# Performance work log

Hardware: AMD Instinct MI355X
Metric: run time of the kernel (lower is better)

Reference implementation:

```python
import jax, jax.numpy as jnp
import numpy as np

B, L, D, A = 4, 4096, 256, 64  # batch, seq_len, n_embd, att_size

def setup_inputs() -> dict:
    key = jax.random.key(0)
    kx, kq, kk, kv = jax.random.split(key, 4)
    x = jax.random.normal(kx, (B, L, D), dtype=jnp.float32)
    # torch nn.Linear(n_embd, att_size) weight is [att_size, n_embd]; we store transposed [D, A]
    s = 1.0 / np.sqrt(D)
    Wq = jax.random.normal(kq, (D, A), dtype=jnp.float32) * s
    Wk = jax.random.normal(kk, (D, A), dtype=jnp.float32) * s
    Wv = jax.random.normal(kv, (D, A), dtype=jnp.float32) * s
    return {"x": x, "Wq": Wq, "Wk": Wk, "Wv": Wv}

def reference(x, Wq, Wk, Wv):
    # q,k,v: [B,L,A]
    q = jnp.einsum('bld,da->bla', x, Wq)
    k = jnp.einsum('bld,da->bla', x, Wk)
    v = jnp.einsum('bld,da->bla', x, Wv)
    # NOTE: original module does NOT scale by 1/sqrt(att_size)
    scores = jnp.einsum('bqa,bka->bqk', q, k)  # [B,L,L]
    Lq = x.shape[1]
    causal = jnp.tril(jnp.ones((Lq, Lq), dtype=bool))
    scores = jnp.where(causal, scores, -jnp.inf)
    weights = jax.nn.softmax(scores, axis=-1)
    # dropout is identity in eval mode
    out = jnp.einsum('bqk,bka->bqa', weights, v)  # [B,L,A]
    return out
```

## Files before the change

### kernel.cpp

```cpp
#include <hip/hip_runtime.h>
#include <math.h>

#define B_ 4
#define L_ 4096
#define D_ 256
#define A_ 64
#define M_ (B_*L_)

typedef _Float16 half4 __attribute__((ext_vector_type(4)));
typedef _Float16 half8 __attribute__((ext_vector_type(8)));
typedef __attribute__((ext_vector_type(4))) float floatx4;

__device__ __forceinline__ unsigned short f2h_(float f) {
    _Float16 h = (_Float16)f;
    return __builtin_bit_cast(unsigned short, h);
}

__global__ __launch_bounds__(256) void wconv_kernel(
    const float* __restrict__ Wq, const float* __restrict__ Wk,
    const float* __restrict__ Wv, unsigned short* __restrict__ wt)
{
    const int w = blockIdx.x, t = threadIdx.x;
    const float* W = (w == 0) ? Wq : (w == 1) ? Wk : Wv;
    unsigned short* o = wt + w * A_ * D_;
    const float scale = (w == 0) ? 1.44269504f : 1.0f;
    __shared__ float T[A_ * 260];
    #pragma unroll
    for (int p = 0; p < 16; ++p) {
        int idx = p * 256 + t;
        int d = idx >> 4, a4 = (idx & 15) * 4;
        float4 v = *(const float4*)(W + d * A_ + a4);
        T[(a4 + 0) * 260 + d] = v.x * scale;
        T[(a4 + 1) * 260 + d] = v.y * scale;
        T[(a4 + 2) * 260 + d] = v.z * scale;
        T[(a4 + 3) * 260 + d] = v.w * scale;
    }
    __syncthreads();
    const int a = t >> 2, d0 = (t & 3) * 64;
    #pragma unroll
    for (int i = 0; i < 16; ++i) {
        float4 v = *(const float4*)(&T[a * 260 + d0 + 4 * i]);
        ushort4 s;
        s.x = f2h_(v.x); s.y = f2h_(v.y); s.z = f2h_(v.z); s.w = f2h_(v.w);
        *(ushort4*)(o + a * D_ + d0 + 4 * i) = s;
    }
}

__global__ __launch_bounds__(384) void proj_kernel(
    const float* __restrict__ x,
    const unsigned short* __restrict__ wt,
    unsigned short* __restrict__ qo,
    unsigned short* __restrict__ ko,
    unsigned short* __restrict__ vto)
{
    __shared__ __align__(16) unsigned short Xh[32 * 264];
    __shared__ __align__(16) unsigned short Cst[6 * 1536];
    const int t = threadIdx.x, m0 = blockIdx.x * 32;

    #pragma unroll
    for (int p = 0; p < 6; ++p) {
        int idx = p * 384 + t;
        if (idx < 2048) {
            int row = idx >> 6, col = (idx & 63) * 4;
            float4 v = *(const float4*)(x + (size_t)(m0 + row) * D_ + col);
            ushort4 s;
            s.x = f2h_(v.x); s.y = f2h_(v.y); s.z = f2h_(v.z); s.w = f2h_(v.w);
            *(ushort4*)(Xh + row * 264 + col) = s;
        }
    }
    __syncthreads();

    const int wid = t >> 6, lane = t & 63, c = lane & 15, g = lane >> 4;
    const int w = wid >> 1, mt = wid & 1;

    half8 xa[8];
    #pragma unroll
    for (int s = 0; s < 8; ++s)
        xa[s] = *(const half8*)(Xh + (16 * mt + c) * 264 + 32 * s + 8 * g);

    const unsigned short* wsrc = wt + w * A_ * D_;
    unsigned short* Cw = Cst + wid * 1536;
    #pragma unroll
    for (int nt = 0; nt < 4; ++nt) {
        floatx4 acc = {0.f, 0.f, 0.f, 0.f};
        #pragma unroll
        for (int s = 0; s < 8; ++s) {
            half8 wb = *(const half8*)(wsrc + (16 * nt + c) * D_ + 32 * s + 8 * g);
            acc = __builtin_amdgcn_mfma_f32_16x16x32_f16(xa[s], wb, acc, 0, 0, 0);
        }
        if (w < 2) {
            #pragma unroll
            for (int r = 0; r < 4; ++r)
                Cw[(4 * g + r) * 72 + 16 * nt + c] = f2h_(acc[r]);
        } else {
            #pragma unroll
            for (int r = 0; r < 4; ++r)
                Cw[(16 * nt + c) * 24 + 4 * g + r] = f2h_(acc[r]);
        }
    }

    if (w < 2) {
        unsigned short* o = (w == 0) ? qo : ko;
        const int row16 = lane >> 2, seg = lane & 3;
        uint4 d0 = *(const uint4*)(Cw + row16 * 72 + seg * 16);
        uint4 d1 = *(const uint4*)(Cw + row16 * 72 + seg * 16 + 8);
        unsigned short* p = o + (size_t)(m0 + 16 * mt + row16) * A_ + seg * 16;
        *(uint4*)(p) = d0;
        *(uint4*)(p + 8) = d1;
    }
    __syncthreads();
    if (t < 256) {
        const int a = t >> 2, quarter = t & 3;
        const int o = quarter * 8, mtv = o >> 4, idx = o & 15;
        uint4 d = *(const uint4*)(Cst + (4 + mtv) * 1536 + a * 24 + idx);
        const int bb = m0 >> 12, l0 = m0 & (L_ - 1);
        *(uint4*)(vto + ((size_t)(bb * A_ + a)) * L_ + l0 + o) = d;
    }
}

__global__ __launch_bounds__(512) void attn_kernel(
    const unsigned short* __restrict__ qb,
    const unsigned short* __restrict__ kb,
    const unsigned short* __restrict__ vt,
    float* __restrict__ poB,
    float2* __restrict__ mlB)
{
    __shared__ __align__(16) unsigned short smem[4 * 4608];
    unsigned short* Ks = smem;
    unsigned short* Vs = smem + 2 * 4608;

    const int t    = threadIdx.x;
    const int lane = t & 63;
    const int wid  = t >> 6;
    const int qsub = wid >> 1;
    const int ph   = wid & 1;
    const int c    = lane & 15;
    const int g    = lane >> 4;

    const int bx = blockIdx.x;
    const int x  = bx & 7, u = bx >> 3;
    const int b  = x >> 1;
    const int gch = 287 - (2 * u + (x & 1));
    int m = 0;
    while (4 * (m + 1) * (m + 2) <= gch) ++m;
    const int rem = gch - 4 * m * (m + 1);
    const int nch = m + 1;
    const int qt  = 8 * m + rem / nch;
    const int j   = rem % nch;
    const int T   = qt + 1;
    const int t0  = (j * T) / nch;
    const int t1  = ((j + 1) * T) / nch;
    const int nIt = (t1 - t0 + 1) >> 1;
    const int Tm1 = T - 1;

    const int q0    = qt * 64;
    const int qrow0 = q0 + 16 * qsub;
    const int qme   = qrow0 + c;

    const size_t base  = (size_t)b * L_ * A_;
    const size_t vbase = (size_t)b * A_ * L_;

    half8 qf[2];
    {
        const unsigned short* qp = qb + base + (size_t)(qrow0 + c) * A_ + g * 8;
        qf[0] = *(const half8*)(qp);
        qf[1] = *(const half8*)(qp + 32);
    }

    floatx4 O4[4];
    #pragma unroll
    for (int at = 0; at < 4; ++at) O4[at] = (floatx4){0.f, 0.f, 0.f, 0.f};
    float m_ = -INFINITY, l_ = 0.f;

    for (int it = 0; it < nIt; ++it) {
        __syncthreads();
        #pragma unroll
        for (int tile = 0; tile < 2; ++tile) {
            const int kts = t0 + 2 * it + tile;
            if (kts < t1) {
                const int k0s = kts << 6;
                const int row = t >> 3, c8 = t & 7;
                uint4 dK = *(const uint4*)(kb + base + (size_t)k0s * 64 + t * 8);
                *(uint4*)(Ks + tile * 4608 + row * 72 + c8 * 8) = dK;
                uint4 dV = *(const uint4*)(vt + vbase + (size_t)row * L_ + k0s + c8 * 8);
                *(uint4*)(Vs + tile * 4608 + row * 72 + c8 * 8) = dV;
            }
        }
        __syncthreads();

        const int kt = t0 + 2 * it + ph;
        if (kt >= t1) continue;
        const int k0 = kt << 6;
        const unsigned short* Kw = Ks + ph * 4608;
        const unsigned short* Vw = Vs + ph * 4608;

        floatx4 S4[4];
        #pragma unroll
        for (int nt = 0; nt < 4; ++nt) S4[nt] = (floatx4){0.f, 0.f, 0.f, 0.f};
        #pragma unroll
        for (int s = 0; s < 2; ++s)
            #pragma unroll
            for (int nt = 0; nt < 4; ++nt) {
                half8 kf = *(const half8*)(Kw + (16 * nt + c) * 72 + 32 * s + 8 * g);
                S4[nt] = __builtin_amdgcn_mfma_f32_16x16x32_f16(kf, qf[s], S4[nt], 0, 0, 0);
            }

        if (kt == Tm1) {
            #pragma unroll
            for (int nt = 0; nt < 4; ++nt)
                #pragma unroll
                for (int r = 0; r < 4; ++r)
                    if (k0 + 16 * nt + 4 * g + r > qme) S4[nt][r] = -INFINITY;
        }

        float tm = fmaxf(fmaxf(fmaxf(S4[0][0], S4[0][1]), fmaxf(S4[0][2], S4[0][3])),
                         fmaxf(fmaxf(S4[1][0], S4[1][1]), fmaxf(S4[1][2], S4[1][3])));
        tm = fmaxf(tm, fmaxf(fmaxf(fmaxf(S4[2][0], S4[2][1]), fmaxf(S4[2][2], S4[2][3])),
                             fmaxf(fmaxf(S4[3][0], S4[3][1]), fmaxf(S4[3][2], S4[3][3]))));
        tm = fmaxf(tm, __shfl_xor(tm, 16));
        tm = fmaxf(tm, __shfl_xor(tm, 32));
        const float mn  = fmaxf(m_, tm);
        const float mnc = fmaxf(mn, -3.0e38f);
        const float al  = exp2f(fminf(m_ - mnc, 0.f));
        float rs = 0.f;
        half4 pf[4];
        #pragma unroll
        for (int nt = 0; nt < 4; ++nt) {
            #pragma unroll
            for (int r = 0; r < 4; ++r) {
                float p = exp2f(S4[nt][r] - mnc);
                S4[nt][r] = p;
                rs += p;
            }
            pf[nt][0] = (_Float16)S4[nt][0];
            pf[nt][1] = (_Float16)S4[nt][1];
            pf[nt][2] = (_Float16)S4[nt][2];
            pf[nt][3] = (_Float16)S4[nt][3];
        }
        rs += __shfl_xor(rs, 16);
        rs += __shfl_xor(rs, 32);
        l_ = l_ * al + rs;
        m_ = mn;

        #pragma unroll
        for (int at = 0; at < 4; ++at) {
            O4[at] *= al;
            #pragma unroll
            for (int nt = 0; nt < 4; ++nt) {
                half4 va = *(const half4*)(Vw + (16 * at + c) * 72 + 16 * nt + 4 * g);
                O4[at] = __builtin_amdgcn_mfma_f32_16x16x16f16(va, pf[nt], O4[at], 0, 0, 0);
            }
        }
    }

    __syncthreads();
    float*  Of  = (float*)smem;
    float2* mlb = (float2*)(smem + 16384);
    #pragma unroll
    for (int at = 0; at < 4; ++at) {
        float4 v; v.x = O4[at][0]; v.y = O4[at][1]; v.z = O4[at][2]; v.w = O4[at][3];
        ((float4*)Of)[wid * 256 + at * 64 + lane] = v;
    }
    if (g == 0) { float2 ml; ml.x = m_; ml.y = l_; mlb[wid * 16 + c] = ml; }
    __syncthreads();

    {
        const int q64 = t >> 3, seg = t & 7;
        const int qs = q64 >> 4, cc = q64 & 15;
        const float2 A0 = mlb[(2 * qs) * 16 + cc];
        const float2 A1 = mlb[(2 * qs + 1) * 16 + cc];
        const float mf = fmaxf(A0.x, A1.x);
        const float mc = fmaxf(mf, -3.0e38f);
        const float w0 = exp2f(A0.x - mc);
        const float w1 = exp2f(A1.x - mc);
        const float ls = w0 * A0.y + w1 * A1.y;
        float res[8];
        #pragma unroll
        for (int u2 = 0; u2 < 8; ++u2) {
            const int a = seg * 8 + u2;
            const int at = a >> 4, gg = (a >> 2) & 3, r = a & 3;
            const int i0 = ((2 * qs) * 256 + at * 64 + gg * 16 + cc) * 4 + r;
            const int i1 = ((2 * qs + 1) * 256 + at * 64 + gg * 16 + cc) * 4 + r;
            res[u2] = w0 * Of[i0] + w1 * Of[i1];
        }
        float* p = poB + (size_t)j * M_ * A_ + base + (size_t)(q0 + q64) * A_ + seg * 8;
        *(float4*)(p)     = make_float4(res[0], res[1], res[2], res[3]);
        *(float4*)(p + 4) = make_float4(res[4], res[5], res[6], res[7]);
        if (seg == 0) {
            float2 ml; ml.x = mf; ml.y = ls;
            mlB[(size_t)j * M_ + b * L_ + q0 + q64] = ml;
        }
    }
}

__global__ __launch_bounds__(256) void merge_kernel(
    float* __restrict__ out, const float* __restrict__ poB,
    const float2* __restrict__ mlB)
{
    const int tg = blockIdx.x * 256 + threadIdx.x;
    const int q = tg >> 4;
    const int qt = (q & (L_ - 1)) >> 6;
    const int nch = (qt + 8) >> 3;
    float2 a[8];
    float mf = -INFINITY;
    for (int jj = 0; jj < nch; ++jj) {
        a[jj] = mlB[(size_t)jj * M_ + q];
        mf = fmaxf(mf, a[jj].x);
    }
    const float mc = fmaxf(mf, -3.0e38f);
    float den = 0.f;
    float4 acc = make_float4(0.f, 0.f, 0.f, 0.f);
    for (int jj = 0; jj < nch; ++jj) {
        const float wj = exp2f(a[jj].x - mc);
        den += wj * a[jj].y;
        const float4 o = ((const float4*)(poB + (size_t)jj * M_ * A_))[tg];
        acc.x += o.x * wj; acc.y += o.y * wj;
        acc.z += o.z * wj; acc.w += o.w * wj;
    }
    const float inv = 1.f / den;
    float4 r;
    r.x = acc.x * inv; r.y = acc.y * inv; r.z = acc.z * inv; r.w = acc.w * inv;
    ((float4*)out)[tg] = r;
}

extern "C" void kernel_launch(void* const* d_in, const int* in_sizes, int n_in,
                              void* d_out, int out_size, void* d_ws, size_t ws_size,
                              hipStream_t stream) {
    const float* x  = (const float*)d_in[0];
    const float* Wq = (const float*)d_in[1];
    const float* Wk = (const float*)d_in[2];
    const float* Wv = (const float*)d_in[3];

    char* ws = (char*)d_ws;
    unsigned short* qb = (unsigned short*)(ws);
    unsigned short* kb = (unsigned short*)(ws + (2u << 20));
    unsigned short* vt = (unsigned short*)(ws + (4u << 20));
    unsigned short* wt = (unsigned short*)(ws + (6u << 20));
    char* p0 = ws + (6u << 20) + (128u << 10);
    float*  poB = (float*)(p0);
    float2* mlB = (float2*)(p0 + (32u << 20));
    float* out = (float*)d_out;

    hipLaunchKernelGGL(wconv_kernel, dim3(3), dim3(256), 0, stream, Wq, Wk, Wv, wt);
    hipLaunchKernelGGL(proj_kernel, dim3(M_ / 32), dim3(384), 0, stream, x, wt, qb, kb, vt);
    hipLaunchKernelGGL(attn_kernel, dim3(1152), dim3(512), 0, stream,
                       qb, kb, vt, poB, mlB);
    hipLaunchKernelGGL(merge_kernel, dim3(1024), dim3(256), 0, stream,
                       out, poB, mlB);
}
```

Before: 147.6 us.

## Process 128-row query tiles per block to reuse K/V tiles across two query fragments

Doubles the query tile from 64 to 128 rows. Each wave now holds two 16-row query fragments, so every K/V tile loaded into shared memory and every V fragment read is used for twice as many queries. The work decomposition is retuned to fewer chunks per tile and half as many blocks, and the merge kernel uses an online rescaling loop with a fixed unroll. This cuts global and LDS traffic per query but raises register pressure (a launch_bounds occupancy hint was added), reduces the number of blocks, and makes the causal-mask path run on two diagonal tiles.

Result: faster. 123.6 us (-16.3%).

```diff
diff --git a/kernel.cpp b/kernel.cpp
--- a/kernel.cpp
+++ b/kernel.cpp
@@ -118,7 +118,7 @@
     }
 }
 
-__global__ __launch_bounds__(512) void attn_kernel(
+__global__ __launch_bounds__(512, 4) void attn_kernel(
     const unsigned short* __restrict__ qb,
     const unsigned short* __restrict__ kb,
     const unsigned short* __restrict__ vt,
@@ -140,37 +140,41 @@
     const int bx = blockIdx.x;
     const int x  = bx & 7, u = bx >> 3;
     const int b  = x >> 1;
-    const int gch = 287 - (2 * u + (x & 1));
+    const int gch = 143 - (2 * u + (x & 1));
     int m = 0;
-    while (4 * (m + 1) * (m + 2) <= gch) ++m;
-    const int rem = gch - 4 * m * (m + 1);
+    while (2 * (m + 1) * (m + 2) <= gch) ++m;
+    const int rem = gch - 2 * m * (m + 1);
     const int nch = m + 1;
-    const int qt  = 8 * m + rem / nch;
+    const int qt  = 4 * m + rem / nch;
     const int j   = rem % nch;
-    const int T   = qt + 1;
+    const int T   = 2 * qt + 2;
     const int t0  = (j * T) / nch;
     const int t1  = ((j + 1) * T) / nch;
     const int nIt = (t1 - t0 + 1) >> 1;
-    const int Tm1 = T - 1;
-
-    const int q0    = qt * 64;
-    const int qrow0 = q0 + 16 * qsub;
-    const int qme   = qrow0 + c;
+    const int Tm2 = T - 2;
+
+    const int q0    = qt * 128;
+    const int qrow0 = q0 + 32 * qsub;
+    const int qme0  = qrow0 + c;
 
     const size_t base  = (size_t)b * L_ * A_;
     const size_t vbase = (size_t)b * A_ * L_;
 
-    half8 qf[2];
-    {
-        const unsigned short* qp = qb + base + (size_t)(qrow0 + c) * A_ + g * 8;
-        qf[0] = *(const half8*)(qp);
-        qf[1] = *(const half8*)(qp + 32);
-    }
-
-    floatx4 O4[4];
-    #pragma unroll
-    for (int at = 0; at < 4; ++at) O4[at] = (floatx4){0.f, 0.f, 0.f, 0.f};
-    float m_ = -INFINITY, l_ = 0.f;
+    half8 qf[2][2];
+    #pragma unroll
+    for (int f = 0; f < 2; ++f) {
+        const unsigned short* qp = qb + base + (size_t)(qrow0 + 16 * f + c) * A_ + g * 8;
+        qf[f][0] = *(const half8*)(qp);
+        qf[f][1] = *(const half8*)(qp + 32);
+    }
+
+    floatx4 O4[2][4];
+    #pragma unroll
+    for (int f = 0; f < 2; ++f)
+        #pragma unroll
+        for (int at = 0; at < 4; ++at) O4[f][at] = (floatx4){0.f, 0.f, 0.f, 0.f};
+    float m_[2] = {-INFINITY, -INFINITY};
+    float l_[2] = {0.f, 0.f};
 
     for (int it = 0; it < nIt; ++it) {
         __syncthreads();
@@ -194,79 +198,88 @@
         const unsigned short* Kw = Ks + ph * 4608;
         const unsigned short* Vw = Vs + ph * 4608;
 
-        floatx4 S4[4];
-        #pragma unroll
-        for (int nt = 0; nt < 4; ++nt) S4[nt] = (floatx4){0.f, 0.f, 0.f, 0.f};
-        #pragma unroll
-        for (int s = 0; s < 2; ++s)
+        half4 pf[2][4];
+        #pragma unroll
+        for (int f = 0; f < 2; ++f) {
+            floatx4 S4[4];
+            #pragma unroll
+            for (int nt = 0; nt < 4; ++nt) S4[nt] = (floatx4){0.f, 0.f, 0.f, 0.f};
+            #pragma unroll
+            for (int s = 0; s < 2; ++s)
+                #pragma unroll
+                for (int nt = 0; nt < 4; ++nt) {
+                    half8 kf = *(const half8*)(Kw + (16 * nt + c) * 72 + 32 * s + 8 * g);
+                    S4[nt] = __builtin_amdgcn_mfma_f32_16x16x32_f16(kf, qf[f][s], S4[nt], 0, 0, 0);
+                }
+
+            if (kt >= Tm2) {
+                const int qme = qme0 + 16 * f;
+                #pragma unroll
+                for (int nt = 0; nt < 4; ++nt)
+                    #pragma unroll
+                    for (int r = 0; r < 4; ++r)
+                        if (k0 + 16 * nt + 4 * g + r > qme) S4[nt][r] = -INFINITY;
+            }
+
+            float tm = fmaxf(fmaxf(fmaxf(S4[0][0], S4[0][1]), fmaxf(S4[0][2], S4[0][3])),
+                             fmaxf(fmaxf(S4[1][0], S4[1][1]), fmaxf(S4[1][2], S4[1][3])));
+            tm = fmaxf(tm, fmaxf(fmaxf(fmaxf(S4[2][0], S4[2][1]), fmaxf(S4[2][2], S4[2][3])),
+                                 fmaxf(fmaxf(S4[3][0], S4[3][1]), fmaxf(S4[3][2], S4[3][3]))));
+            tm = fmaxf(tm, __shfl_xor(tm, 16));
+            tm = fmaxf(tm, __shfl_xor(tm, 32));
+            const float mn  = fmaxf(m_[f], tm);
+            const float mnc = fmaxf(mn, -3.0e38f);
+            const float al  = exp2f(fminf(m_[f] - mnc, 0.f));
+            float rs = 0.f;
             #pragma unroll
             for (int nt = 0; nt < 4; ++nt) {
-                half8 kf = *(const half8*)(Kw + (16 * nt + c) * 72 + 32 * s + 8 * g);
-                S4[nt] = __builtin_amdgcn_mfma_f32_16x16x32_f16(kf, qf[s], S4[nt], 0, 0, 0);
+                #pragma unroll
+                for (int r = 0; r < 4; ++r) {
+                    float p = exp2f(S4[nt][r] - mnc);
+                    S4[nt][r] = p;
+                    rs += p;
+                }
+                pf[f][nt][0] = (_Float16)S4[nt][0];
+                pf[f][nt][1] = (_Float16)S4[nt][1];
+                pf[f][nt][2] = (_Float16)S4[nt][2];
+                pf[f][nt][3] = (_Float16)S4[nt][3];
             }
-
-        if (kt == Tm1) {
-            #pragma unroll
-            for (int nt = 0; nt < 4; ++nt)
-                #pragma unroll
-                for (int r = 0; r < 4; ++r)
-                    if (k0 + 16 * nt + 4 * g + r > qme) S4[nt][r] = -INFINITY;
-        }
-
-        float tm = fmaxf(fmaxf(fmaxf(S4[0][0], S4[0][1]), fmaxf(S4[0][2], S4[0][3])),
-                         fmaxf(fmaxf(S4[1][0], S4[1][1]), fmaxf(S4[1][2], S4[1][3])));
-        tm = fmaxf(tm, fmaxf(fmaxf(fmaxf(S4[2][0], S4[2][1]), fmaxf(S4[2][2], S4[2][3])),
-                             fmaxf(fmaxf(S4[3][0], S4[3][1]), fmaxf(S4[3][2], S4[3][3]))));
-        tm = fmaxf(tm, __shfl_xor(tm, 16));
-        tm = fmaxf(tm, __shfl_xor(tm, 32));
-        const float mn  = fmaxf(m_, tm);
-        const float mnc = fmaxf(mn, -3.0e38f);
-        const float al  = exp2f(fminf(m_ - mnc, 0.f));
-        float rs = 0.f;
-        half4 pf[4];
-        #pragma unroll
-        for (int nt = 0; nt < 4; ++nt) {
-            #pragma unroll
-            for (int r = 0; r < 4; ++r) {
-                float p = exp2f(S4[nt][r] - mnc);
-                S4[nt][r] = p;
-                rs += p;
-            }
-            pf[nt][0] = (_Float16)S4[nt][0];
-            pf[nt][1] = (_Float16)S4[nt][1];
-            pf[nt][2] = (_Float16)S4[nt][2];
-            pf[nt][3] = (_Float16)S4[nt][3];
-        }
-        rs += __shfl_xor(rs, 16);
-        rs += __shfl_xor(rs, 32);
-        l_ = l_ * al + rs;
-        m_ = mn;
+            rs += __shfl_xor(rs, 16);
+            rs += __shfl_xor(rs, 32);
+            l_[f] = l_[f] * al + rs;
+            m_[f] = mn;
+            #pragma unroll
+            for (int at = 0; at < 4; ++at) O4[f][at] *= al;
+        }
 
         #pragma unroll
         for (int at = 0; at < 4; ++at) {
-            O4[at] *= al;
             #pragma unroll
             for (int nt = 0; nt < 4; ++nt) {
                 half4 va = *(const half4*)(Vw + (16 * at + c) * 72 + 16 * nt + 4 * g);
-                O4[at] = __builtin_amdgcn_mfma_f32_16x16x16f16(va, pf[nt], O4[at], 0, 0, 0);
+                O4[0][at] = __builtin_amdgcn_mfma_f32_16x16x16f16(va, pf[0][nt], O4[0][at], 0, 0, 0);
+                O4[1][at] = __builtin_amdgcn_mfma_f32_16x16x16f16(va, pf[1][nt], O4[1][at], 0, 0, 0);
             }
         }
     }
 
-    __syncthreads();
     float*  Of  = (float*)smem;
     float2* mlb = (float2*)(smem + 16384);
     #pragma unroll
-    for (int at = 0; at < 4; ++at) {
-        float4 v; v.x = O4[at][0]; v.y = O4[at][1]; v.z = O4[at][2]; v.w = O4[at][3];
-        ((float4*)Of)[wid * 256 + at * 64 + lane] = v;
-    }
-    if (g == 0) { float2 ml; ml.x = m_; ml.y = l_; mlb[wid * 16 + c] = ml; }
-    __syncthreads();
-
-    {
+    for (int f = 0; f < 2; ++f) {
+        __syncthreads();
+        #pragma unroll
+        for (int at = 0; at < 4; ++at) {
+            float4 v; v.x = O4[f][at][0]; v.y = O4[f][at][1];
+            v.z = O4[f][at][2]; v.w = O4[f][at][3];
+            ((float4*)Of)[wid * 256 + at * 64 + lane] = v;
+        }
+        if (g == 0) { float2 ml; ml.x = m_[f]; ml.y = l_[f]; mlb[wid * 16 + c] = ml; }
+        __syncthreads();
+
         const int q64 = t >> 3, seg = t & 7;
         const int qs = q64 >> 4, cc = q64 & 15;
+        const int rowq = 32 * qs + 16 * f + cc;
         const float2 A0 = mlb[(2 * qs) * 16 + cc];
         const float2 A1 = mlb[(2 * qs + 1) * 16 + cc];
         const float mf = fmaxf(A0.x, A1.x);
@@ -283,12 +296,12 @@
             const int i1 = ((2 * qs + 1) * 256 + at * 64 + gg * 16 + cc) * 4 + r;
             res[u2] = w0 * Of[i0] + w1 * Of[i1];
         }
-        float* p = poB + (size_t)j * M_ * A_ + base + (size_t)(q0 + q64) * A_ + seg * 8;
+        float* p = poB + (size_t)j * M_ * A_ + base + (size_t)(q0 + rowq) * A_ + seg * 8;
         *(float4*)(p)     = make_float4(res[0], res[1], res[2], res[3]);
         *(float4*)(p + 4) = make_float4(res[4], res[5], res[6], res[7]);
         if (seg == 0) {
             float2 ml; ml.x = mf; ml.y = ls;
-            mlB[(size_t)j * M_ + b * L_ + q0 + q64] = ml;
+            mlB[(size_t)j * M_ + b * L_ + q0 + rowq] = ml;
         }
     }
 }
@@ -299,23 +312,26 @@
 {
     const int tg = blockIdx.x * 256 + threadIdx.x;
     const int q = tg >> 4;
-    const int qt = (q & (L_ - 1)) >> 6;
-    const int nch = (qt + 8) >> 3;
-    float2 a[8];
-    float mf = -INFINITY;
-    for (int jj = 0; jj < nch; ++jj) {
-        a[jj] = mlB[(size_t)jj * M_ + q];
-        mf = fmaxf(mf, a[jj].x);
-    }
-    const float mc = fmaxf(mf, -3.0e38f);
-    float den = 0.f;
+    const int qt = (q & (L_ - 1)) >> 7;
+    const int nch = (qt + 4) >> 2;
+    float mf = -INFINITY, den = 0.f;
     float4 acc = make_float4(0.f, 0.f, 0.f, 0.f);
-    for (int jj = 0; jj < nch; ++jj) {
-        const float wj = exp2f(a[jj].x - mc);
-        den += wj * a[jj].y;
-        const float4 o = ((const float4*)(poB + (size_t)jj * M_ * A_))[tg];
-        acc.x += o.x * wj; acc.y += o.y * wj;
-        acc.z += o.z * wj; acc.w += o.w * wj;
+    #pragma unroll
+    for (int jj = 0; jj < 8; ++jj) {
+        if (jj < nch) {
+            const float2 aj = mlB[(size_t)jj * M_ + q];
+            const float mn = fmaxf(mf, aj.x);
+            const float mc = fmaxf(mn, -3.0e38f);
+            const float sc = exp2f(fminf(mf - mc, 0.f));
+            const float wj = exp2f(aj.x - mc);
+            const float4 o = ((const float4*)(poB + (size_t)jj * M_ * A_))[tg];
+            acc.x = acc.x * sc + o.x * wj;
+            acc.y = acc.y * sc + o.y * wj;
+            acc.z = acc.z * sc + o.z * wj;
+            acc.w = acc.w * sc + o.w * wj;
+            den = den * sc + aj.y * wj;
+            mf = mn;
+        }
     }
     const float inv = 1.f / den;
     float4 r;
@@ -343,7 +359,7 @@
 
     hipLaunchKernelGGL(wconv_kernel, dim3(3), dim3(256), 0, stream, Wq, Wk, Wv, wt);
     hipLaunchKernelGGL(proj_kernel, dim3(M_ / 32), dim3(384), 0, stream, x, wt, qb, kb, vt);
-    hipLaunchKernelGGL(attn_kernel, dim3(1152), dim3(512), 0, stream,
+    hipLaunchKernelGGL(attn_kernel, dim3(576), dim3(512), 0, stream,
                        qb, kb, vt, poB, mlB);
     hipLaunchKernelGGL(merge_kernel, dim3(1024), dim3(256), 0, stream,
                        out, poB, mlB);
```
